# Performance work log

Measured on AMD Instinct MI355X. Metric: run time of the kernel, lower is better.

## Reference

```python
import jax, jax.numpy as jnp
import numpy as np

# dims
B, L = 2, 1024            # batch, seq len (queries == keys)
DQ, DK, DSRC = 1024, 1024, 512
VIEWS, WIDTH, TOPK = 8, 4, 8
DVP = DQ // VIEWS         # per-view head dim = 128
PAD_F = (WIDTH - 1) // 2  # dilocal 'same' zero padding (stride=1, dilation=1)
PAD_B = (WIDTH - 1) - PAD_F


def setup_inputs() -> dict:
    key = jax.random.key(0)
    ks = jax.random.split(key, 5)
    s = 0.02
    return {
        "query": jax.random.normal(ks[0], (B, L, DQ), jnp.float32),
        "key_t": jax.random.normal(ks[1], (B, L, DK), jnp.float32),
        "source": jax.random.normal(ks[2], (B, L, DSRC), jnp.float32),
        "wq": jax.random.normal(ks[3], (VIEWS, DVP, DQ), jnp.float32) * s,
        "bq": jnp.zeros((VIEWS, DVP), jnp.float32),
        "wk": jax.random.normal(ks[4], (VIEWS, DVP, DK), jnp.float32) * s,
        "bk": jnp.zeros((VIEWS, DVP), jnp.float32),
    }


def reference(query, key_t, source, wq, bq, wk, bk):
    # --- ViewPointFactory.forward ---
    # multi-view projections: [B, L, D] -> [B, views, L, dvp]
    q = jnp.einsum('bld,vkd->bvlk', query, wq) + bq[None, :, None, :]
    k = jnp.einsum('bld,vkd->bvlk', key_t, wk) + bk[None, :, None, :]
    # attention scores over all keys: [B, views, Lq, Lk] (no sqrt(d) scaling in source)
    score = jnp.einsum('bvqd,bvkd->bvqk', q, k)
    # torch.sort(descending) + slice == top_k with sorted values
    vals, idx = jax.lax.top_k(score, TOPK)          # [B, views, Lq, TOPK]
    weights = jax.nn.softmax(vals, axis=-1)

    # --- ViewPoint.__call__(source) ---
    # dilocal: width-WIDTH local windows, stride 1, dilation 1, zero 'same' pad
    padded = jnp.pad(source, ((0, 0), (PAD_F, PAD_B), (0, 0)))
    win_idx = jnp.arange(L)[:, None] + jnp.arange(WIDTH)[None, :]  # [L, WIDTH]
    windows = padded[:, win_idx, :]                 # [B, L, WIDTH, DSRC]

    # gather the top-k key windows per (view, query): [B, views, Lq, TOPK, WIDTH, DSRC]
    gathered = jax.vmap(lambda w, i: w[i])(windows, idx)
    # weighted sum over top-k -> [B, views, Lq, WIDTH, DSRC]
    out = jnp.einsum('bvqk,bvqkwd->bvqwd', weights, gathered)
    return out
```

## Files before the change

### kernel.cpp

```cpp
#include <hip/hip_runtime.h>
#include <cstdint>

#define L_SEQ 1024
#define DSRC 512
#define XPL 2097152L
#define WPL 1048576L

typedef __attribute__((ext_vector_type(8))) short short8;
typedef __attribute__((ext_vector_type(4))) float floatx4;

__device__ __forceinline__ unsigned short f2bf(float f) {
  unsigned int x = __float_as_uint(f);
  x += 0x7fff + ((x >> 16) & 1);
  return (unsigned short)(x >> 16);
}
__device__ __forceinline__ float bf2f(unsigned short h) {
  return __uint_as_float((unsigned)h << 16);
}
__device__ __forceinline__ void split3(float f, unsigned short* h) {
  h[0] = f2bf(f);
  float d = f - bf2f(h[0]);
  h[1] = f2bf(d);
  h[2] = f2bf(d - bf2f(h[1]));
}

__global__ __launch_bounds__(256) void split_inputs_k(
    const float* __restrict__ query, const float* __restrict__ key_t,
    const float* __restrict__ wq, const float* __restrict__ wk,
    ushort* __restrict__ xs, ushort* __restrict__ wsp) {
  int blk = blockIdx.x;
  const float* in; ushort* out; long pl; int idx;
  if (blk < 2048)      { in = query; out = xs;           pl = XPL; idx = blk; }
  else if (blk < 4096) { in = key_t; out = xs + 3 * XPL; pl = XPL; idx = blk - 2048; }
  else if (blk < 5120) { in = wq;    out = wsp;          pl = WPL; idx = blk - 4096; }
  else                 { in = wk;    out = wsp + 3 * WPL; pl = WPL; idx = blk - 5120; }
  long e = (long)idx * 1024 + threadIdx.x * 4;
  float4 v = *(const float4*)(in + e);
  unsigned short h0[3], h1[3], h2[3], h3[3];
  split3(v.x, h0); split3(v.y, h1); split3(v.z, h2); split3(v.w, h3);
#pragma unroll
  for (int s = 0; s < 3; s++) {
    ushort4 u; u.x = h0[s]; u.y = h1[s]; u.z = h2[s]; u.w = h3[s];
    *(ushort4*)(out + s * pl + e) = u;
  }
}

__global__ __launch_bounds__(512) void proj_gemm_k(
    const ushort* __restrict__ xs, const ushort* __restrict__ wsp,
    float* __restrict__ C, const float* __restrict__ bq, const float* __restrict__ bk) {
  __shared__ ushort As[3][4096];
  __shared__ ushort Bs[3][4096];
  int z = blockIdx.z;
  const ushort* Ab = xs + (long)z * 3 * XPL + (long)blockIdx.y * 128 * 1024;
  const ushort* Bb = wsp + (long)z * 3 * WPL + (long)blockIdx.x * 128 * 1024;
  const float* bias = z ? bk : bq;

  int tid = threadIdx.x;
  int lane = tid & 63, wv = tid >> 6;
  int wm = wv >> 2, wn = wv & 3;
  int quad = lane >> 4, l16 = lane & 15;

  int sr = tid >> 2;
  int sc = (tid & 3) * 8;

  floatx4 acc[4][2] = {};

  for (int k0 = 0; k0 < 1024; k0 += 32) {
    short8 ga[3], gb[3];
#pragma unroll
    for (int s = 0; s < 3; s++) {
      ga[s] = *(const short8*)(Ab + s * XPL + (long)sr * 1024 + k0 + sc);
      gb[s] = *(const short8*)(Bb + s * WPL + (long)sr * 1024 + k0 + sc);
    }
    __syncthreads();
#pragma unroll
    for (int s = 0; s < 3; s++) {
      *(short8*)(&As[s][sr * 32 + sc]) = ga[s];
      *(short8*)(&Bs[s][sr * 32 + sc]) = gb[s];
    }
    __syncthreads();

    short8 af[3][4];
#pragma unroll
    for (int s = 0; s < 3; s++)
#pragma unroll
      for (int i = 0; i < 4; i++)
        af[s][i] = *(const short8*)(&As[s][(wm * 64 + i * 16 + l16) * 32 + quad * 8]);
#pragma unroll
    for (int j = 0; j < 2; j++) {
      int boff = (wn * 32 + j * 16 + l16) * 32 + quad * 8;
      short8 b0 = *(const short8*)(&Bs[0][boff]);
      short8 b1 = *(const short8*)(&Bs[1][boff]);
      short8 b2 = *(const short8*)(&Bs[2][boff]);
#pragma unroll
      for (int i = 0; i < 4; i++) {
        acc[i][j] = __builtin_amdgcn_mfma_f32_16x16x32_bf16(af[1][i], b1, acc[i][j], 0, 0, 0);
        acc[i][j] = __builtin_amdgcn_mfma_f32_16x16x32_bf16(af[0][i], b2, acc[i][j], 0, 0, 0);
        acc[i][j] = __builtin_amdgcn_mfma_f32_16x16x32_bf16(af[2][i], b0, acc[i][j], 0, 0, 0);
        acc[i][j] = __builtin_amdgcn_mfma_f32_16x16x32_bf16(af[0][i], b1, acc[i][j], 0, 0, 0);
        acc[i][j] = __builtin_amdgcn_mfma_f32_16x16x32_bf16(af[1][i], b0, acc[i][j], 0, 0, 0);
        acc[i][j] = __builtin_amdgcn_mfma_f32_16x16x32_bf16(af[0][i], b0, acc[i][j], 0, 0, 0);
      }
    }
  }

  float* Cb = C + (long)z * XPL;
#pragma unroll
  for (int j = 0; j < 2; j++) {
    int col = blockIdx.x * 128 + wn * 32 + j * 16 + l16;
    float bv = bias[col];
#pragma unroll
    for (int i = 0; i < 4; i++) {
#pragma unroll
      for (int r = 0; r < 4; r++) {
        int row = blockIdx.y * 128 + wm * 64 + i * 16 + quad * 4 + r;
        Cb[(long)row * 1024 + col] = acc[i][j][r] + bv;
      }
    }
  }
}

__global__ __launch_bounds__(256) void score_gemm_k(
    const float* __restrict__ qp, const float* __restrict__ kp,
    float* __restrict__ S) {
  __shared__ ushort As[3][4096];
  __shared__ ushort Bs[3][4096];
  int z = blockIdx.z;
  int b = z >> 3, v = z & 7;
  const float* Aq = qp + (long)b * 1048576 + v * 128 + (long)blockIdx.y * 128 * 1024;
  const float* Bq = kp + (long)b * 1048576 + v * 128 + (long)blockIdx.x * 128 * 1024;

  int tid = threadIdx.x;
  int lane = tid & 63, wv = tid >> 6;
  int wm = wv >> 1, wn = wv & 1;
  int quad = lane >> 4, l16 = lane & 15;

  int sr = tid >> 3;
  int sc4 = (tid & 7) * 4;

  floatx4 acc[4][4] = {};

  for (int k0 = 0; k0 < 128; k0 += 32) {
    float4 av[4], bv4[4];
#pragma unroll
    for (int it = 0; it < 4; it++) {
      av[it] = *(const float4*)(Aq + (long)(sr + 32 * it) * 1024 + k0 + sc4);
      bv4[it] = *(const float4*)(Bq + (long)(sr + 32 * it) * 1024 + k0 + sc4);
    }
    __syncthreads();
#pragma unroll
    for (int it = 0; it < 4; it++) {
      int r = sr + 32 * it;
      const float* afp = (const float*)&av[it];
      const float* bfp = (const float*)&bv4[it];
      unsigned short ha[4][3], hb[4][3];
#pragma unroll
      for (int e = 0; e < 4; e++) { split3(afp[e], ha[e]); split3(bfp[e], hb[e]); }
#pragma unroll
      for (int s = 0; s < 3; s++) {
        ushort4 ua; ua.x = ha[0][s]; ua.y = ha[1][s]; ua.z = ha[2][s]; ua.w = ha[3][s];
        ushort4 ub; ub.x = hb[0][s]; ub.y = hb[1][s]; ub.z = hb[2][s]; ub.w = hb[3][s];
        *(ushort4*)(&As[s][r * 32 + sc4]) = ua;
        *(ushort4*)(&Bs[s][r * 32 + sc4]) = ub;
      }
    }
    __syncthreads();

    short8 af[3][4];
#pragma unroll
    for (int s = 0; s < 3; s++)
#pragma unroll
      for (int i = 0; i < 4; i++)
        af[s][i] = *(const short8*)(&As[s][(wm * 64 + i * 16 + l16) * 32 + quad * 8]);
#pragma unroll
    for (int j = 0; j < 4; j++) {
      int boff = (wn * 64 + j * 16 + l16) * 32 + quad * 8;
      short8 b0 = *(const short8*)(&Bs[0][boff]);
      short8 b1 = *(const short8*)(&Bs[1][boff]);
      short8 b2 = *(const short8*)(&Bs[2][boff]);
#pragma unroll
      for (int i = 0; i < 4; i++) {
        acc[i][j] = __builtin_amdgcn_mfma_f32_16x16x32_bf16(af[1][i], b1, acc[i][j], 0, 0, 0);
        acc[i][j] = __builtin_amdgcn_mfma_f32_16x16x32_bf16(af[0][i], b2, acc[i][j], 0, 0, 0);
        acc[i][j] = __builtin_amdgcn_mfma_f32_16x16x32_bf16(af[2][i], b0, acc[i][j], 0, 0, 0);
        acc[i][j] = __builtin_amdgcn_mfma_f32_16x16x32_bf16(af[0][i], b1, acc[i][j], 0, 0, 0);
        acc[i][j] = __builtin_amdgcn_mfma_f32_16x16x32_bf16(af[1][i], b0, acc[i][j], 0, 0, 0);
        acc[i][j] = __builtin_amdgcn_mfma_f32_16x16x32_bf16(af[0][i], b0, acc[i][j], 0, 0, 0);
      }
    }
  }

  float* Sb = S + (long)z * 1048576;
#pragma unroll
  for (int j = 0; j < 4; j++) {
    int col = blockIdx.x * 128 + wn * 64 + j * 16 + l16;
#pragma unroll
    for (int i = 0; i < 4; i++) {
#pragma unroll
      for (int r = 0; r < 4; r++) {
        int row = blockIdx.y * 128 + wm * 64 + i * 16 + quad * 4 + r;
        Sb[(long)row * 1024 + col] = acc[i][j][r];
      }
    }
  }
}

__global__ __launch_bounds__(256) void topk_softmax_k(const float* __restrict__ scores,
                                                      float* __restrict__ wts,
                                                      int* __restrict__ idxs) {
  int row = blockIdx.x * 4 + (threadIdx.x >> 6);
  int lane = threadIdx.x & 63;
  const float* s = scores + (long)row * 1024;
  float v[16];
#pragma unroll
  for (int i = 0; i < 16; i++) v[i] = s[lane + i * 64];

  float topv[8]; int topi[8];
  for (int t = 0; t < 8; t++) {
    float bv = -1e30f; int bi = 1 << 30; int bslot = -1;
#pragma unroll
    for (int i = 0; i < 16; i++) {
      int ci = lane + i * 64;
      if (v[i] > bv) { bv = v[i]; bi = ci; bslot = i; }
    }
    float rv = bv; int ri = bi;
    for (int off = 32; off; off >>= 1) {
      float ov = __shfl_down(rv, off);
      int oi = __shfl_down(ri, off);
      if (ov > rv || (ov == rv && oi < ri)) { rv = ov; ri = oi; }
    }
    rv = __shfl(rv, 0); ri = __shfl(ri, 0);
    topv[t] = rv; topi[t] = ri;
    if (bslot >= 0 && bi == ri) v[bslot] = -1e30f;
  }
  float m = topv[0], sum = 0.f, e[8];
#pragma unroll
  for (int t = 0; t < 8; t++) { e[t] = __expf(topv[t] - m); sum += e[t]; }
  float inv = 1.0f / sum;
  if (lane < 8) {
    wts[(long)row * 8 + lane] = e[lane] * inv;
    idxs[(long)row * 8 + lane] = topi[lane];
  }
}

__global__ __launch_bounds__(256) void gather_out_k(const float* __restrict__ src,
                                                    const float* __restrict__ wts,
                                                    const int* __restrict__ idxs,
                                                    float* __restrict__ out) {
  int rowid = blockIdx.x;
  int b = rowid >> 13;
  int tid = threadIdx.x;
  int d4 = tid & 127;
  int w0 = (tid >> 7) << 1;
  const float4* s4 = (const float4*)src + (long)b * (L_SEQ * (DSRC / 4));
  float wt[8]; int id[8];
#pragma unroll
  for (int k = 0; k < 8; k++) {
    wt[k] = wts[(long)rowid * 8 + k];
    id[k] = idxs[(long)rowid * 8 + k];
  }
  float ax = 0, ay = 0, az = 0, aw = 0;
  float bx = 0, by = 0, bz2 = 0, bw = 0;
#pragma unroll
  for (int k = 0; k < 8; k++) {
    int r0 = id[k] + w0 - 1;
    if ((unsigned)r0 < (unsigned)L_SEQ) {
      float4 x = s4[(long)r0 * 128 + d4];
      ax += wt[k] * x.x; ay += wt[k] * x.y; az += wt[k] * x.z; aw += wt[k] * x.w;
    }
    int r1 = r0 + 1;
    if ((unsigned)r1 < (unsigned)L_SEQ) {
      float4 x = s4[(long)r1 * 128 + d4];
      bx += wt[k] * x.x; by += wt[k] * x.y; bz2 += wt[k] * x.z; bw += wt[k] * x.w;
    }
  }
  float4* o4 = (float4*)out + ((long)rowid * 4 + w0) * 128 + d4;
  o4[0] = make_float4(ax, ay, az, aw);
  o4[128] = make_float4(bx, by, bz2, bw);
}

extern "C" void kernel_launch(void* const* d_in, const int* in_sizes, int n_in,
                              void* d_out, int out_size, void* d_ws, size_t ws_size,
                              hipStream_t stream) {
  (void)in_sizes; (void)n_in; (void)out_size; (void)ws_size;
  const float* query  = (const float*)d_in[0];
  const float* key_t  = (const float*)d_in[1];
  const float* source = (const float*)d_in[2];
  const float* wq     = (const float*)d_in[3];
  const float* bq     = (const float*)d_in[4];
  const float* wk     = (const float*)d_in[5];
  const float* bk     = (const float*)d_in[6];

  char* ws = (char*)d_ws;
  float* qp   = (float*)(ws + 0);
  float* kp   = (float*)(ws + 8388608);
  float* wts  = (float*)(ws + 16777216);
  int*   idxs = (int*)(ws + 17301504);
  ushort* xs  = (ushort*)(ws + 17825792);
  ushort* wsp = (ushort*)(ws + 17825792 + 25165824);
  float* sc   = (float*)(ws + 17825792);

  split_inputs_k<<<6144, 256, 0, stream>>>(query, key_t, wq, wk, xs, wsp);
  proj_gemm_k<<<dim3(8, 16, 2), 512, 0, stream>>>(xs, wsp, qp, bq, bk);
  score_gemm_k<<<dim3(8, 8, 16), 256, 0, stream>>>(qp, kp, sc);
  topk_softmax_k<<<4096, 256, 0, stream>>>(sc, wts, idxs);
  gather_out_k<<<16384, 256, 0, stream>>>(source, wts, idxs, (float*)d_out);
}
```

Measured before the change: 325.8 us.

## Emit split bf16 projections and stage GEMM tiles via global_load_lds

The projection GEMM now writes its output already split into three bf16 planes, so the score GEMM loads bf16 tiles directly and no longer re-splits fp32 values per tile. Both GEMMs stage tiles with the direct global-to-LDS load builtin instead of going through registers. The projection tile shrinks to 128x64 with 256 threads, and the score plus top-k stages are split per batch so the workspace fits. In exchange the projection output triples in size in bf16 form, there are more kernel launches, and the direct-to-LDS path adds an extra barrier per k-step.

New measurement: 328.4 us. About the same (+0.8%).

```diff
diff --git a/kernel.cpp b/kernel.cpp
--- a/kernel.cpp
+++ b/kernel.cpp
@@ -22,6 +22,13 @@
   float d = f - bf2f(h[0]);
   h[1] = f2bf(d);
   h[2] = f2bf(d - bf2f(h[1]));
+}
+
+__device__ __forceinline__ void gll16(const void* g, void* l) {
+  __builtin_amdgcn_global_load_lds(
+      (const __attribute__((address_space(1))) void*)(uintptr_t)g,
+      (__attribute__((address_space(3))) void*)(uint32_t)(uintptr_t)l,
+      16, 0, 0);
 }
 
 __global__ __launch_bounds__(256) void split_inputs_k(
@@ -30,9 +37,9 @@
     ushort* __restrict__ xs, ushort* __restrict__ wsp) {
   int blk = blockIdx.x;
   const float* in; ushort* out; long pl; int idx;
-  if (blk < 2048)      { in = query; out = xs;           pl = XPL; idx = blk; }
-  else if (blk < 4096) { in = key_t; out = xs + 3 * XPL; pl = XPL; idx = blk - 2048; }
-  else if (blk < 5120) { in = wq;    out = wsp;          pl = WPL; idx = blk - 4096; }
+  if (blk < 2048)      { in = query; out = xs;            pl = XPL; idx = blk; }
+  else if (blk < 4096) { in = key_t; out = xs + 3 * XPL;  pl = XPL; idx = blk - 2048; }
+  else if (blk < 5120) { in = wq;    out = wsp;           pl = WPL; idx = blk - 4096; }
   else                 { in = wk;    out = wsp + 3 * WPL; pl = WPL; idx = blk - 5120; }
   long e = (long)idx * 1024 + threadIdx.x * 4;
   float4 v = *(const float4*)(in + e);
@@ -45,38 +52,38 @@
   }
 }
 
-__global__ __launch_bounds__(512) void proj_gemm_k(
+__global__ __launch_bounds__(256) void proj_gemm_k(
     const ushort* __restrict__ xs, const ushort* __restrict__ wsp,
-    float* __restrict__ C, const float* __restrict__ bq, const float* __restrict__ bk) {
+    ushort* __restrict__ out, const float* __restrict__ bq, const float* __restrict__ bk) {
   __shared__ ushort As[3][4096];
-  __shared__ ushort Bs[3][4096];
+  __shared__ ushort Bs[3][2048];
   int z = blockIdx.z;
-  const ushort* Ab = xs + (long)z * 3 * XPL + (long)blockIdx.y * 128 * 1024;
-  const ushort* Bb = wsp + (long)z * 3 * WPL + (long)blockIdx.x * 128 * 1024;
+  const ushort* Ag = xs + (long)z * 3 * XPL + (long)blockIdx.y * 128 * 1024;
+  const ushort* Bg = wsp + (long)z * 3 * WPL + (long)blockIdx.x * 64 * 1024;
   const float* bias = z ? bk : bq;
 
   int tid = threadIdx.x;
   int lane = tid & 63, wv = tid >> 6;
-  int wm = wv >> 2, wn = wv & 3;
+  int wm = wv >> 1, wn = wv & 1;
   int quad = lane >> 4, l16 = lane & 15;
 
-  int sr = tid >> 2;
-  int sc = (tid & 3) * 8;
+  int srow = lane >> 2;
+  int scol = (lane & 3) * 8;
 
   floatx4 acc[4][2] = {};
 
   for (int k0 = 0; k0 < 1024; k0 += 32) {
-    short8 ga[3], gb[3];
 #pragma unroll
     for (int s = 0; s < 3; s++) {
-      ga[s] = *(const short8*)(Ab + s * XPL + (long)sr * 1024 + k0 + sc);
-      gb[s] = *(const short8*)(Bb + s * WPL + (long)sr * 1024 + k0 + sc);
-    }
-    __syncthreads();
-#pragma unroll
-    for (int s = 0; s < 3; s++) {
-      *(short8*)(&As[s][sr * 32 + sc]) = ga[s];
-      *(short8*)(&Bs[s][sr * 32 + sc]) = gb[s];
+#pragma unroll
+      for (int c = 0; c < 2; c++) {
+        int r0 = wv * 32 + c * 16;
+        gll16(Ag + (long)s * XPL + (long)(r0 + srow) * 1024 + k0 + scol,
+              &As[s][r0 * 32]);
+      }
+      int r0b = wv * 16;
+      gll16(Bg + (long)s * WPL + (long)(r0b + srow) * 1024 + k0 + scol,
+            &Bs[s][r0b * 32]);
     }
     __syncthreads();
 
@@ -102,66 +109,57 @@
         acc[i][j] = __builtin_amdgcn_mfma_f32_16x16x32_bf16(af[0][i], b0, acc[i][j], 0, 0, 0);
       }
     }
-  }
-
-  float* Cb = C + (long)z * XPL;
+    __syncthreads();
+  }
+
+  ushort* Pg = out + (long)z * 3 * XPL;
 #pragma unroll
   for (int j = 0; j < 2; j++) {
-    int col = blockIdx.x * 128 + wn * 32 + j * 16 + l16;
+    int col = blockIdx.x * 64 + wn * 32 + j * 16 + l16;
     float bv = bias[col];
 #pragma unroll
     for (int i = 0; i < 4; i++) {
 #pragma unroll
       for (int r = 0; r < 4; r++) {
         int row = blockIdx.y * 128 + wm * 64 + i * 16 + quad * 4 + r;
-        Cb[(long)row * 1024 + col] = acc[i][j][r] + bv;
+        unsigned short h[3];
+        split3(acc[i][j][r] + bv, h);
+#pragma unroll
+        for (int s = 0; s < 3; s++)
+          Pg[(long)s * XPL + (long)row * 1024 + col] = h[s];
       }
     }
   }
 }
 
 __global__ __launch_bounds__(256) void score_gemm_k(
-    const float* __restrict__ qp, const float* __restrict__ kp,
-    float* __restrict__ S) {
+    const ushort* __restrict__ ps, float* __restrict__ S, int b) {
   __shared__ ushort As[3][4096];
   __shared__ ushort Bs[3][4096];
-  int z = blockIdx.z;
-  int b = z >> 3, v = z & 7;
-  const float* Aq = qp + (long)b * 1048576 + v * 128 + (long)blockIdx.y * 128 * 1024;
-  const float* Bq = kp + (long)b * 1048576 + v * 128 + (long)blockIdx.x * 128 * 1024;
+  int v = blockIdx.z;
+  const ushort* Ag = ps + (long)(b * 1024 + blockIdx.y * 128) * 1024 + v * 128;
+  const ushort* Bg = ps + 3 * XPL + (long)(b * 1024 + blockIdx.x * 128) * 1024 + v * 128;
 
   int tid = threadIdx.x;
   int lane = tid & 63, wv = tid >> 6;
   int wm = wv >> 1, wn = wv & 1;
   int quad = lane >> 4, l16 = lane & 15;
 
-  int sr = tid >> 3;
-  int sc4 = (tid & 7) * 4;
+  int srow = lane >> 2;
+  int scol = (lane & 3) * 8;
 
   floatx4 acc[4][4] = {};
 
   for (int k0 = 0; k0 < 128; k0 += 32) {
-    float4 av[4], bv4[4];
-#pragma unroll
-    for (int it = 0; it < 4; it++) {
-      av[it] = *(const float4*)(Aq + (long)(sr + 32 * it) * 1024 + k0 + sc4);
-      bv4[it] = *(const float4*)(Bq + (long)(sr + 32 * it) * 1024 + k0 + sc4);
-    }
-    __syncthreads();
-#pragma unroll
-    for (int it = 0; it < 4; it++) {
-      int r = sr + 32 * it;
-      const float* afp = (const float*)&av[it];
-      const float* bfp = (const float*)&bv4[it];
-      unsigned short ha[4][3], hb[4][3];
-#pragma unroll
-      for (int e = 0; e < 4; e++) { split3(afp[e], ha[e]); split3(bfp[e], hb[e]); }
-#pragma unroll
-      for (int s = 0; s < 3; s++) {
-        ushort4 ua; ua.x = ha[0][s]; ua.y = ha[1][s]; ua.z = ha[2][s]; ua.w = ha[3][s];
-        ushort4 ub; ub.x = hb[0][s]; ub.y = hb[1][s]; ub.z = hb[2][s]; ub.w = hb[3][s];
-        *(ushort4*)(&As[s][r * 32 + sc4]) = ua;
-        *(ushort4*)(&Bs[s][r * 32 + sc4]) = ub;
+#pragma unroll
+    for (int s = 0; s < 3; s++) {
+#pragma unroll
+      for (int c = 0; c < 2; c++) {
+        int r0 = wv * 32 + c * 16;
+        gll16(Ag + (long)s * XPL + (long)(r0 + srow) * 1024 + k0 + scol,
+              &As[s][r0 * 32]);
+        gll16(Bg + (long)s * XPL + (long)(r0 + srow) * 1024 + k0 + scol,
+              &Bs[s][r0 * 32]);
       }
     }
     __syncthreads();
@@ -188,9 +186,10 @@
         acc[i][j] = __builtin_amdgcn_mfma_f32_16x16x32_bf16(af[0][i], b0, acc[i][j], 0, 0, 0);
       }
     }
-  }
-
-  float* Sb = S + (long)z * 1048576;
+    __syncthreads();
+  }
+
+  float* Sb = S + (long)v * 1048576;
 #pragma unroll
   for (int j = 0; j < 4; j++) {
     int col = blockIdx.x * 128 + wn * 64 + j * 16 + l16;
@@ -292,17 +291,19 @@
   const float* bk     = (const float*)d_in[6];
 
   char* ws = (char*)d_ws;
-  float* qp   = (float*)(ws + 0);
-  float* kp   = (float*)(ws + 8388608);
-  float* wts  = (float*)(ws + 16777216);
-  int*   idxs = (int*)(ws + 17301504);
-  ushort* xs  = (ushort*)(ws + 17825792);
-  ushort* wsp = (ushort*)(ws + 17825792 + 25165824);
-  float* sc   = (float*)(ws + 17825792);
+  ushort* xs  = (ushort*)(ws + 0);
+  ushort* wsp = (ushort*)(ws + 25165824);
+  float*  sc  = (float*)(ws + 0);
+  ushort* qs  = (ushort*)(ws + 37748736);
+  float*  wts = (float*)(ws + 62914560);
+  int*   idxs = (int*)(ws + 63438848);
 
   split_inputs_k<<<6144, 256, 0, stream>>>(query, key_t, wq, wk, xs, wsp);
-  proj_gemm_k<<<dim3(8, 16, 2), 512, 0, stream>>>(xs, wsp, qp, bq, bk);
-  score_gemm_k<<<dim3(8, 8, 16), 256, 0, stream>>>(qp, kp, sc);
-  topk_softmax_k<<<4096, 256, 0, stream>>>(sc, wts, idxs);
+  proj_gemm_k<<<dim3(16, 16, 2), 256, 0, stream>>>(xs, wsp, qs, bq, bk);
+  for (int b = 0; b < 2; b++) {
+    score_gemm_k<<<dim3(8, 8, 8), 256, 0, stream>>>(qs, sc, b);
+    topk_softmax_k<<<2048, 256, 0, stream>>>(sc, wts + (long)b * 65536,
+                                             idxs + (long)b * 65536);
+  }
   gather_out_k<<<16384, 256, 0, stream>>>(source, wts, idxs, (float*)d_out);
 }
```
